# Kernel optimization log

Hardware: AMD Instinct MI355X
Metric: run time of the kernel (lower is better)

## Reference

```python
import jax, jax.numpy as jnp
import numpy as np

N_SPK, M_UTT, D_EMB = 8192, 10, 128
CLAMP_MIN = 1e-6


def setup_inputs() -> dict:
    key = jax.random.key(0)
    x = jax.random.normal(key, (N_SPK, M_UTT, D_EMB), dtype=jnp.float32)
    w = jnp.asarray(10.0, dtype=jnp.float32)   # learned scale (init_w)
    b = jnp.asarray(-5.0, dtype=jnp.float32)   # learned bias  (init_b)
    return {"x": x, "w": w, "b": b}


def reference(x, w, b):
    # x: [N, M, D]. Faithful to the torch module:
    #   - centroids = mean over all M utterances per speaker
    #   - calc_new_centroids replaces speaker's own centroid with mean(dvecs[spkr,:M]),
    #     which IS the full centroid -> new_centroids == centroids (no-op, kept faithful)
    #   - only the last utterance (utt_indx == M-1) contributes a row -> [N, 1, N]
    n, m, d = x.shape
    centroids = jnp.mean(x, axis=1)                       # [N, D]
    last = x[:, m - 1, :]                                 # [N, D] last utterance per speaker
    num = jnp.einsum('nd,kd->nk', last, centroids)        # [N, N]
    denom = (jnp.linalg.norm(last, axis=1)[:, None]
             * jnp.linalg.norm(centroids, axis=1)[None, :])
    cos_sim = jnp.clip(num / denom, CLAMP_MIN)            # torch.clamp(x, 1e-6) = min-clamp
    logits = cos_sim * w + b                              # [N, N] (view(-1, N) with M=1)
    # CrossEntropyLoss with labels arange(N) (repeat_interleave with M=1 is identity)
    logp = jax.nn.log_softmax(logits, axis=-1)
    labels = jnp.arange(n)
    loss = -jnp.mean(jnp.take_along_axis(logp, labels[:, None], axis=1))
    return loss
```

## Files before the change

### kernel.cpp

```cpp
#include <hip/hip_runtime.h>
#include <hip/hip_bf16.h>


typedef __attribute__((ext_vector_type(8))) short short8;
typedef __attribute__((ext_vector_type(4))) float f32x4;

#define NSPK 8192
#define DEMB 128
#define MUTT 10
#define LOG2E 1.44269504088896340736f
#define LN2   0.69314718055994530942f

#define WS_ZDIAG 0
#define WS_ZSUM  8192
#define WS_LASTB 65536
#define WS_CENTB 2162688

__global__ __launch_bounds__(256) void k1_prep(const float* __restrict__ x,
                                               const float* __restrict__ wp,
                                               float* __restrict__ W,
                                               __hip_bfloat16* __restrict__ lastb,
                                               __hip_bfloat16* __restrict__ centb) {
    const int wv = threadIdx.x >> 6;
    const int l  = threadIdx.x & 63;
    const int n  = blockIdx.x * 4 + wv;
    if (blockIdx.x < 32) W[WS_ZSUM + blockIdx.x * 256 + threadIdx.x] = 0.f;

    const float* xr = x + (size_t)n * (MUTT * DEMB) + 2 * l;
    float sx = 0.f, sy = 0.f, vx = 0.f, vy = 0.f;
#pragma unroll
    for (int m = 0; m < MUTT; ++m) {
        float2 t = *(const float2*)(xr + m * DEMB);
        vx = t.x; vy = t.y; sx += t.x; sy += t.y;
    }
    const float cx = sx * 0.1f, cy = sy * 0.1f;
    float sl = vx * vx + vy * vy;
    float sc = cx * cx + cy * cy;
    float dp = vx * cx + vy * cy;
#pragma unroll
    for (int off = 1; off < 64; off <<= 1) {
        sl += __shfl_xor(sl, off);
        sc += __shfl_xor(sc, off);
        dp += __shfl_xor(dp, off);
    }
    const float il = rsqrtf(sl), ic = rsqrtf(sc);
    const float scale = wp[0] * LOG2E;
    const float as = il * scale;
    __hip_bfloat162 lv, cv;
    lv.x = __float2bfloat16(vx * as); lv.y = __float2bfloat16(vy * as);
    cv.x = __float2bfloat16(cx * ic); cv.y = __float2bfloat16(cy * ic);
    *(__hip_bfloat162*)(lastb + n * DEMB + 2 * l) = lv;
    *(__hip_bfloat162*)(centb + n * DEMB + 2 * l) = cv;
    if (l == 0) {
        const float lo = scale >= 0.f ? 1e-6f * scale : -INFINITY;
        const float hi = scale >= 0.f ? INFINITY : 1e-6f * scale;
        W[WS_ZDIAG + n] = fminf(fmaxf(dp * il * ic * scale, lo), hi);
    }
}

__global__ __launch_bounds__(256, 2) void k2_main(
        const __hip_bfloat16* __restrict__ lastb,
        const __hip_bfloat16* __restrict__ centb,
        const float* __restrict__ wp,
        float* __restrict__ W) {
    const int tid  = threadIdx.x;
    const int lane = tid & 63;
    const int wv   = tid >> 6;
    const int quad = lane >> 4;
    const int l16  = lane & 15;
    const int R0   = blockIdx.x * 256;
    const int C0   = blockIdx.y * 512;
    const float scale = wp[0] * LOG2E;
    const float c0  = __builtin_amdgcn_exp2f(1e-6f * scale);
    const float elo = scale >= 0.f ? c0 : 0.f;
    const float ehi = scale >= 0.f ? INFINITY : c0;

    __shared__ uint4 Bs4[2048];
    char* Bsc = (char*)Bs4;

    const int srow = wv * 16 + quad;
    const int sp   = l16;

#pragma unroll
    for (int i = 0; i < 4; ++i) {
        const int row = srow + i * 4;
        const int c   = sp ^ (row & 15);
        const char* src = (const char*)centb + ((size_t)(C0 + row) << 8) + (c << 4);
        char* dst = Bsc + (wv * 4096 + i * 1024 + lane * 16);
        __builtin_amdgcn_global_load_lds(
            (const __attribute__((address_space(1))) unsigned int*)src,
            (__attribute__((address_space(3))) unsigned int*)dst, 16, 0, 0);
    }

    short8 a[4][4];
    {
        const short* ap = (const short*)lastb + (size_t)(R0 + wv * 64 + l16) * DEMB + quad * 8;
#pragma unroll
        for (int rt = 0; rt < 4; ++rt)
#pragma unroll
            for (int kc = 0; kc < 4; ++kc)
                a[rt][kc] = *(const short8*)(ap + rt * 16 * DEMB + kc * 32);
    }

    int roff[4];
#pragma unroll
    for (int kc = 0; kc < 4; ++kc)
        roff[kc] = l16 * 256 + (((quad + 4 * kc) ^ l16) << 4);

    float racc[4][4] = {{0.f}};

    for (int it = 0; it < 8; ++it) {
        __syncthreads();
        if (it < 7) {
            const int c0n = C0 + (it + 1) * 64;
            char* bufn = Bsc + ((it + 1) & 1) * 16384;
#pragma unroll
            for (int i = 0; i < 4; ++i) {
                const int row = srow + i * 4;
                const int c   = sp ^ (row & 15);
                const char* src = (const char*)centb + ((size_t)(c0n + row) << 8) + (c << 4);
                char* dst = bufn + (wv * 4096 + i * 1024 + lane * 16);
                __builtin_amdgcn_global_load_lds(
                    (const __attribute__((address_space(1))) unsigned int*)src,
                    (__attribute__((address_space(3))) unsigned int*)dst, 16, 0, 0);
            }
        }
        const char* buf = Bsc + (it & 1) * 16384;
#pragma unroll
        for (int nt = 0; nt < 4; ++nt) {
            short8 b[4];
#pragma unroll
            for (int kc = 0; kc < 4; ++kc)
                b[kc] = *(const short8*)(buf + nt * 4096 + roff[kc]);
#pragma unroll
            for (int rt = 0; rt < 4; ++rt) {
                f32x4 acc = {0.f, 0.f, 0.f, 0.f};
#pragma unroll
                for (int kc = 0; kc < 4; ++kc)
                    acc = __builtin_amdgcn_mfma_f32_16x16x32_bf16(a[rt][kc], b[kc], acc, 0, 0, 0);
#pragma unroll
                for (int r = 0; r < 4; ++r) {
                    const float e = __builtin_amdgcn_exp2f(acc[r]);
                    racc[rt][r] += fminf(fmaxf(e, elo), ehi);
                }
            }
        }
    }
#pragma unroll
    for (int off = 1; off < 16; off <<= 1)
#pragma unroll
        for (int rt = 0; rt < 4; ++rt)
#pragma unroll
            for (int r = 0; r < 4; ++r)
                racc[rt][r] += __shfl_xor(racc[rt][r], off);
    if (l16 == 0) {
#pragma unroll
        for (int rt = 0; rt < 4; ++rt)
#pragma unroll
            for (int r = 0; r < 4; ++r)
                atomicAdd(&W[WS_ZSUM + R0 + wv * 64 + rt * 16 + quad * 4 + r], racc[rt][r]);
    }
}

__global__ __launch_bounds__(256) void k3_loss(const float* __restrict__ W,
                                               float* __restrict__ out) {
    float v = 0.f;
    for (int n = threadIdx.x; n < NSPK; n += 256)
        v += __log2f(W[WS_ZSUM + n]) - W[WS_ZDIAG + n];
#pragma unroll
    for (int off = 1; off < 64; off <<= 1) v += __shfl_xor(v, off);
    __shared__ float red[4];
    if ((threadIdx.x & 63) == 0) red[threadIdx.x >> 6] = v;
    __syncthreads();
    if (threadIdx.x == 0)
        out[0] = (red[0] + red[1] + red[2] + red[3]) * (LN2 / (float)NSPK);
}

extern "C" void kernel_launch(void* const* d_in, const int* in_sizes, int n_in,
                              void* d_out, int out_size, void* d_ws, size_t ws_size,
                              hipStream_t stream) {
    const float* x = (const float*)d_in[0];
    const float* w = (const float*)d_in[1];
    float* W = (float*)d_ws;
    __hip_bfloat16* lastb = (__hip_bfloat16*)((char*)d_ws + WS_LASTB);
    __hip_bfloat16* centb = (__hip_bfloat16*)((char*)d_ws + WS_CENTB);

    k1_prep<<<NSPK / 4, 256, 0, stream>>>(x, w, W, lastb, centb);
    k2_main<<<dim3(32, 16), 256, 0, stream>>>(lastb, centb, w, W);
    k3_loss<<<1, 256, 0, stream>>>(W, (float*)d_out);
}
```

Measured before the change: 114.9 us.

## Fuse loss reduction into GEMM kernel via ticket counter; vectorize prep loads

```diff
diff --git a/kernel.cpp b/kernel.cpp
--- a/kernel.cpp
+++ b/kernel.cpp
@@ -15,6 +15,7 @@
 #define WS_ZSUM  8192
 #define WS_LASTB 65536
 #define WS_CENTB 2162688
+#define WS_TICKET_I 1064960
 
 __global__ __launch_bounds__(256) void k1_prep(const float* __restrict__ x,
                                                const float* __restrict__ wp,
@@ -25,20 +26,39 @@
     const int l  = threadIdx.x & 63;
     const int n  = blockIdx.x * 4 + wv;
     if (blockIdx.x < 32) W[WS_ZSUM + blockIdx.x * 256 + threadIdx.x] = 0.f;
-
-    const float* xr = x + (size_t)n * (MUTT * DEMB) + 2 * l;
-    float sx = 0.f, sy = 0.f, vx = 0.f, vy = 0.f;
-#pragma unroll
-    for (int m = 0; m < MUTT; ++m) {
-        float2 t = *(const float2*)(xr + m * DEMB);
-        vx = t.x; vy = t.y; sx += t.x; sy += t.y;
-    }
-    const float cx = sx * 0.1f, cy = sy * 0.1f;
-    float sl = vx * vx + vy * vy;
-    float sc = cx * cx + cy * cy;
-    float dp = vx * cx + vy * cy;
-#pragma unroll
-    for (int off = 1; off < 64; off <<= 1) {
+    if (blockIdx.x == 32 && threadIdx.x == 0) ((int*)W)[WS_TICKET_I] = 0;
+
+    const float4* xr = (const float4*)(x + (size_t)n * (MUTT * DEMB)) + l;
+    float4 v[5];
+#pragma unroll
+    for (int i = 0; i < 5; ++i) v[i] = xr[i * 64];
+
+    float4 cs;
+    cs.x = ((v[0].x + v[1].x) + (v[2].x + v[3].x)) + v[4].x;
+    cs.y = ((v[0].y + v[1].y) + (v[2].y + v[3].y)) + v[4].y;
+    cs.z = ((v[0].z + v[1].z) + (v[2].z + v[3].z)) + v[4].z;
+    cs.w = ((v[0].w + v[1].w) + (v[2].w + v[3].w)) + v[4].w;
+    cs.x += __shfl_xor(cs.x, 32);
+    cs.y += __shfl_xor(cs.y, 32);
+    cs.z += __shfl_xor(cs.z, 32);
+    cs.w += __shfl_xor(cs.w, 32);
+    float4 cent;
+    cent.x = cs.x * 0.1f; cent.y = cs.y * 0.1f; cent.z = cs.z * 0.1f; cent.w = cs.w * 0.1f;
+
+    float4 lv = v[4];
+    {
+        const float tx = __shfl_xor(lv.x, 32);
+        const float ty = __shfl_xor(lv.y, 32);
+        const float tz = __shfl_xor(lv.z, 32);
+        const float tw = __shfl_xor(lv.w, 32);
+        if (l < 32) { lv.x = tx; lv.y = ty; lv.z = tz; lv.w = tw; }
+    }
+
+    float sl = lv.x * lv.x + lv.y * lv.y + lv.z * lv.z + lv.w * lv.w;
+    float sc = cent.x * cent.x + cent.y * cent.y + cent.z * cent.z + cent.w * cent.w;
+    float dp = lv.x * cent.x + lv.y * cent.y + lv.z * cent.z + lv.w * cent.w;
+#pragma unroll
+    for (int off = 1; off < 32; off <<= 1) {
         sl += __shfl_xor(sl, off);
         sc += __shfl_xor(sc, off);
         dp += __shfl_xor(dp, off);
@@ -46,11 +66,17 @@
     const float il = rsqrtf(sl), ic = rsqrtf(sc);
     const float scale = wp[0] * LOG2E;
     const float as = il * scale;
-    __hip_bfloat162 lv, cv;
-    lv.x = __float2bfloat16(vx * as); lv.y = __float2bfloat16(vy * as);
-    cv.x = __float2bfloat16(cx * ic); cv.y = __float2bfloat16(cy * ic);
-    *(__hip_bfloat162*)(lastb + n * DEMB + 2 * l) = lv;
-    *(__hip_bfloat162*)(centb + n * DEMB + 2 * l) = cv;
+
+    const float  f  = (l < 32) ? as : ic;
+    const float4 s4 = (l < 32) ? lv : cent;
+    __hip_bfloat16* bp = ((l < 32) ? lastb : centb) + (size_t)n * DEMB + 4 * (l & 31);
+    union { __hip_bfloat162 h[2]; uint2 u; } pk;
+    pk.h[0].x = __float2bfloat16(s4.x * f);
+    pk.h[0].y = __float2bfloat16(s4.y * f);
+    pk.h[1].x = __float2bfloat16(s4.z * f);
+    pk.h[1].y = __float2bfloat16(s4.w * f);
+    *(uint2*)bp = pk.u;
+
     if (l == 0) {
         const float lo = scale >= 0.f ? 1e-6f * scale : -INFINITY;
         const float hi = scale >= 0.f ? INFINITY : 1e-6f * scale;
@@ -62,7 +88,8 @@
         const __hip_bfloat16* __restrict__ lastb,
         const __hip_bfloat16* __restrict__ centb,
         const float* __restrict__ wp,
-        float* __restrict__ W) {
+        float* __restrict__ W,
+        float* __restrict__ out) {
     const int tid  = threadIdx.x;
     const int lane = tid & 63;
     const int wv   = tid >> 6;
@@ -72,10 +99,11 @@
     const int C0   = blockIdx.y * 512;
     const float scale = wp[0] * LOG2E;
     const float c0  = __builtin_amdgcn_exp2f(1e-6f * scale);
-    const float elo = scale >= 0.f ? c0 : 0.f;
-    const float ehi = scale >= 0.f ? INFINITY : c0;
+    const bool  pos = (scale >= 0.f);
 
     __shared__ uint4 Bs4[2048];
+    __shared__ int   lastFlag;
+    __shared__ float red[4];
     char* Bsc = (char*)Bs4;
 
     const int srow = wv * 16 + quad;
@@ -132,16 +160,27 @@
 #pragma unroll
             for (int kc = 0; kc < 4; ++kc)
                 b[kc] = *(const short8*)(buf + nt * 4096 + roff[kc]);
-#pragma unroll
-            for (int rt = 0; rt < 4; ++rt) {
-                f32x4 acc = {0.f, 0.f, 0.f, 0.f};
-#pragma unroll
-                for (int kc = 0; kc < 4; ++kc)
-                    acc = __builtin_amdgcn_mfma_f32_16x16x32_bf16(a[rt][kc], b[kc], acc, 0, 0, 0);
-#pragma unroll
-                for (int r = 0; r < 4; ++r) {
-                    const float e = __builtin_amdgcn_exp2f(acc[r]);
-                    racc[rt][r] += fminf(fmaxf(e, elo), ehi);
+            if (pos) {
+#pragma unroll
+                for (int rt = 0; rt < 4; ++rt) {
+                    f32x4 acc = {0.f, 0.f, 0.f, 0.f};
+#pragma unroll
+                    for (int kc = 0; kc < 4; ++kc)
+                        acc = __builtin_amdgcn_mfma_f32_16x16x32_bf16(a[rt][kc], b[kc], acc, 0, 0, 0);
+#pragma unroll
+                    for (int r = 0; r < 4; ++r)
+                        racc[rt][r] += fmaxf(__builtin_amdgcn_exp2f(acc[r]), c0);
+                }
+            } else {
+#pragma unroll
+                for (int rt = 0; rt < 4; ++rt) {
+                    f32x4 acc = {0.f, 0.f, 0.f, 0.f};
+#pragma unroll
+                    for (int kc = 0; kc < 4; ++kc)
+                        acc = __builtin_amdgcn_mfma_f32_16x16x32_bf16(a[rt][kc], b[kc], acc, 0, 0, 0);
+#pragma unroll
+                    for (int r = 0; r < 4; ++r)
+                        racc[rt][r] += fminf(__builtin_amdgcn_exp2f(acc[r]), c0);
                 }
             }
         }
@@ -160,20 +199,30 @@
             for (int r = 0; r < 4; ++r)
                 atomicAdd(&W[WS_ZSUM + R0 + wv * 64 + rt * 16 + quad * 4 + r], racc[rt][r]);
     }
-}
-
-__global__ __launch_bounds__(256) void k3_loss(const float* __restrict__ W,
-                                               float* __restrict__ out) {
-    float v = 0.f;
-    for (int n = threadIdx.x; n < NSPK; n += 256)
-        v += __log2f(W[WS_ZSUM + n]) - W[WS_ZDIAG + n];
-#pragma unroll
-    for (int off = 1; off < 64; off <<= 1) v += __shfl_xor(v, off);
-    __shared__ float red[4];
-    if ((threadIdx.x & 63) == 0) red[threadIdx.x >> 6] = v;
+
+    __threadfence();
     __syncthreads();
-    if (threadIdx.x == 0)
-        out[0] = (red[0] + red[1] + red[2] + red[3]) * (LN2 / (float)NSPK);
+    if (tid == 0) {
+        const int prev = __hip_atomic_fetch_add((int*)W + WS_TICKET_I, 1,
+                                                __ATOMIC_ACQ_REL, __HIP_MEMORY_SCOPE_AGENT);
+        lastFlag = (prev == 32 * 16 - 1);
+    }
+    __syncthreads();
+    if (lastFlag) {
+        __threadfence();
+        float vsum = 0.f;
+        for (int nn = tid; nn < NSPK; nn += 256) {
+            const float s = __hip_atomic_load((const float*)W + WS_ZSUM + nn,
+                                              __ATOMIC_RELAXED, __HIP_MEMORY_SCOPE_AGENT);
+            vsum += __log2f(s) - W[WS_ZDIAG + nn];
+        }
+#pragma unroll
+        for (int off = 1; off < 64; off <<= 1) vsum += __shfl_xor(vsum, off);
+        if ((tid & 63) == 0) red[tid >> 6] = vsum;
+        __syncthreads();
+        if (tid == 0)
+            out[0] = (red[0] + red[1] + red[2] + red[3]) * (LN2 / (float)NSPK);
+    }
 }
 
 extern "C" void kernel_launch(void* const* d_in, const int* in_sizes, int n_in,
@@ -186,6 +235,5 @@
     __hip_bfloat16* centb = (__hip_bfloat16*)((char*)d_ws + WS_CENTB);
 
     k1_prep<<<NSPK / 4, 256, 0, stream>>>(x, w, W, lastb, centb);
-    k2_main<<<dim3(32, 16), 256, 0, stream>>>(lastb, centb, w, W);
-    k3_loss<<<1, 256, 0, stream>>>(W, (float*)d_out);
+    k2_main<<<dim3(32, 16), 256, 0, stream>>>(lastb, centb, w, W, (float*)d_out);
 }
```

Measured after the change: 149.6 us. 30.2% more time.
